# Kernel tuning notes

Measured on AMD Instinct MI355X. Metric: run time of the kernel, lower is better.

## Reference

```python
import jax, jax.numpy as jnp
import numpy as np

TEMPERATURE = 8.0  # sqrt(d_k), d_k=64
NEG_INF = -1e9

def setup_inputs() -> dict:
    key = jax.random.key(0)
    kq, kk, kv, km, kb = jax.random.split(key, 5)
    B, H, L, D = 2, 16, 2048, 64
    q = jax.random.normal(kq, (B, H, L, D), dtype=jnp.float32)
    k = jax.random.normal(kk, (B, H, L, D), dtype=jnp.float32)
    v = jax.random.normal(kv, (B, H, L, D), dtype=jnp.float32)
    mask = jax.random.randint(km, (B, 1, L, L), 0, 2, dtype=jnp.int32)
    pair_bias = jax.random.normal(kb, (B, 1, L, L), dtype=jnp.float32)
    return {"q": q, "k": k, "v": v, "mask": mask, "pair_bias": pair_bias}

def reference(q, k, v, mask, pair_bias):
    # scores: [B, H, Lq, Lk]
    attn = jnp.einsum('bhqd,bhkd->bhqk', q / TEMPERATURE, k)
    attn = attn + pair_bias  # broadcast over heads
    attn = jnp.where(mask == 0, NEG_INF, attn)
    attn = jax.nn.softmax(attn, axis=-1)
    # dropout prob is 0.0 -> identity
    head_output = jnp.einsum('bhqk,bhkd->bhqd', attn, v)
    return (head_output, attn)
```

## Files before the change

### kernel.cpp

```cpp
#include <hip/hip_runtime.h>

#define L  2048
#define D  64
#define NH 16
#define NB 2
#define KT 64
#define NT 32
#define LOG2E 1.44269504088896f

using half8   = _Float16 __attribute__((ext_vector_type(8)));
using half4v  = _Float16 __attribute__((ext_vector_type(4)));
using float4v = float    __attribute__((ext_vector_type(4)));
using int4v   = int      __attribute__((ext_vector_type(4)));

#define BAR()    asm volatile("s_barrier" ::: "memory")
#define WAITV(n) asm volatile("s_waitcnt vmcnt(" #n ")" ::: "memory")
#define WAITL()  asm volatile("s_waitcnt lgkmcnt(0)" ::: "memory")

__device__ __forceinline__ void gload16(const void* g, void* l) {
    __builtin_amdgcn_global_load_lds((const __attribute__((address_space(1))) void*)g,
                                     (__attribute__((address_space(3))) void*)l, 16, 0, 0);
}
__device__ __forceinline__ void gload4(const void* g, void* l) {
    __builtin_amdgcn_global_load_lds((const __attribute__((address_space(1))) void*)g,
                                     (__attribute__((address_space(3))) void*)l, 4, 0, 0);
}

__global__ __launch_bounds__(256) void prep_qk(const float* __restrict__ q,
                                               const float* __restrict__ k,
                                               _Float16* __restrict__ qh,
                                               _Float16* __restrict__ kh) {
    int i = (blockIdx.x * 256 + threadIdx.x) * 8;
    float4v a0 = *(const float4v*)(q + i);
    float4v a1 = *(const float4v*)(q + i + 4);
    float4v b0 = *(const float4v*)(k + i);
    float4v b1 = *(const float4v*)(k + i + 4);
    half8 qo, ko;
    const float s = 0.125f * LOG2E;
#pragma unroll
    for (int j = 0; j < 4; ++j) {
        qo[j]     = (_Float16)(a0[j] * s);
        qo[4 + j] = (_Float16)(a1[j] * s);
        ko[j]     = (_Float16)b0[j];
        ko[4 + j] = (_Float16)b1[j];
    }
    *(half8*)(qh + i) = qo;
    *(half8*)(kh + i) = ko;
}

__global__ __launch_bounds__(256) void prep_vt(const float* __restrict__ v,
                                               _Float16* __restrict__ vt) {
    __shared__ float tile[64][65];
    int bh = blockIdx.x >> 5;
    int l0 = (blockIdx.x & 31) * 64;
    const float* vb = v + (size_t)bh * L * D + (size_t)l0 * D;
    int row = threadIdx.x >> 2, c0 = (threadIdx.x & 3) * 16;
#pragma unroll
    for (int j = 0; j < 16; j += 4) {
        float4v t4 = *(const float4v*)(vb + row * D + c0 + j);
        tile[row][c0 + j + 0] = t4[0];
        tile[row][c0 + j + 1] = t4[1];
        tile[row][c0 + j + 2] = t4[2];
        tile[row][c0 + j + 3] = t4[3];
    }
    __syncthreads();
    int d = threadIdx.x >> 2, kbl = threadIdx.x & 3;
    int lq = kbl * 16;
    _Float16* ob = vt + (((size_t)bh * 128 + (l0 >> 4) + kbl) * 64 + d) * 16;
    half8 o0, o1;
#pragma unroll
    for (int j = 0; j < 8; ++j) {
        o0[j] = (_Float16)tile[lq + j][d];
        o1[j] = (_Float16)tile[lq + 8 + j][d];
    }
    *(half8*)(ob)     = o0;
    *(half8*)(ob + 8) = o1;
}

__global__ __launch_bounds__(256) void prep_mbh(const int* __restrict__ mask,
                                                const float* __restrict__ bias,
                                                _Float16* __restrict__ mbh) {
    int blk = blockIdx.x;
    int bq = blk >> 3, tg = blk & 7;
    int b  = bq >> 7, qt = bq & 127;
    int row = threadIdx.x >> 4;
    int c16 = threadIdx.x & 15;
    const int*   mrow = mask + ((size_t)b * L + qt * 16 + row) * L;
    const float* brow = bias + ((size_t)b * L + qt * 16 + row) * L;
    _Float16* obase = mbh + (size_t)bq * 32768 + (c16 >> 2) * 256 + row * 16 + (c16 & 3) * 4;
#pragma unroll
    for (int tt = 0; tt < 4; ++tt) {
        int t = tg * 4 + tt;
        int key = t * 64 + c16 * 4;
        int4v   m  = *(const int4v*)(mrow + key);
        float4v bb = *(const float4v*)(brow + key);
        half4v o;
        o[0] = m[0] ? (_Float16)(bb[0] * LOG2E) : (_Float16)(-1500.0f);
        o[1] = m[1] ? (_Float16)(bb[1] * LOG2E) : (_Float16)(-1500.0f);
        o[2] = m[2] ? (_Float16)(bb[2] * LOG2E) : (_Float16)(-1500.0f);
        o[3] = m[3] ? (_Float16)(bb[3] * LOG2E) : (_Float16)(-1500.0f);
        *(half4v*)(obase + t * 1024) = o;
    }
}

__global__ __launch_bounds__(256, 4) void attn_fused(const _Float16* __restrict__ qh,
                                                     const _Float16* __restrict__ kh,
                                                     const _Float16* __restrict__ vt,
                                                     const _Float16* __restrict__ mbh,
                                                     float* __restrict__ out_ho,
                                                     float* __restrict__ out_attn) {
    __shared__ __align__(16) char arena[36864];
    __shared__ float lpart[4][16];
    __shared__ float rls[16];

    int p  = blockIdx.x;
    int l  = (p & 7) * 512 + (p >> 3);
    int b  = l >> 11, h = (l >> 7) & 15, qt = l & 127;
    int bh = b * NH + h;
    int q0 = qt * 16;

    int tid = threadIdx.x, w = tid >> 6, lane = tid & 63;
    int cg = lane & 15, grp = lane >> 4;

    const _Float16* kg = kh  + (size_t)bh * L * D;
    const _Float16* vg = vt  + (size_t)bh * 131072;
    const _Float16* mg = mbh + (size_t)(b * 128 + qt) * 32768;
    const _Float16* qg = qh  + ((size_t)bh * L + q0) * D;

    half8 aq0 = *(const half8*)(qg + cg * D + grp * 8);
    half8 aq1 = *(const half8*)(qg + cg * D + 32 + grp * 8);

    _Float16* kbw = (_Float16*)(arena)         + w * 2048;
    _Float16* vbw = (_Float16*)(arena + 16384) + w * 2048;
    _Float16* mbw = (_Float16*)(arena + 32768) + w * 512;

    const int r8  = lane >> 3;
    const int kch = ((lane & 7) ^ r8) * 8;

    auto stage = [&](int t, int bs) {
        int kb = t * 4 + w;
        int k0 = kb * 16;
        _Float16* kd = kbw + bs * 1024;
        gload16(kg + (size_t)(k0 +     r8) * D + kch, kd);
        gload16(kg + (size_t)(k0 + 8 + r8) * D + kch, kd + 512);
        _Float16* vd = vbw + bs * 1024;
        const _Float16* vs = vg + (size_t)kb * 1024;
        gload16(vs + lane * 8, vd);
        gload16(vs + 512 + lane * 8, vd + 512);
        _Float16* md = mbw + bs * 256;
        const _Float16* ms = mg + (size_t)t * 1024 + w * 256;
        gload4(ms + lane * 2, md);
        gload4(ms + 128 + lane * 2, md + 128);
    };

    const int kro = cg * 64;
    const int ks0 = ((grp)     ^ (cg & 7)) * 8;
    const int ks1 = ((4 + grp) ^ (cg & 7)) * 8;
    const int mro = cg * 16 + grp * 4;
    const int vro = grp * 4;

    half4v puh[NT];
    float ls = 0.f;
    float4v oa0 = {0.f,0.f,0.f,0.f}, oa1 = {0.f,0.f,0.f,0.f};
    float4v oa2 = {0.f,0.f,0.f,0.f}, oa3 = {0.f,0.f,0.f,0.f};

    stage(0, 0);
#pragma unroll
    for (int t = 0; t < NT; ++t) {
        const int bs = t & 1;
        if (t + 1 < NT) { stage(t + 1, bs ^ 1); WAITV(6); }
        else            { WAITV(0); }
        const _Float16* kb = kbw + bs * 1024;
        const _Float16* mb = mbw + bs * 256;
        const _Float16* vb = vbw + bs * 1024;
        half8  bk0 = *(const half8*)(kb + kro + ks0);
        half8  bk1 = *(const half8*)(kb + kro + ks1);
        half4v m4  = *(const half4v*)(mb + mro);
        float4v acc;
        acc[0] = (float)m4[0]; acc[1] = (float)m4[1];
        acc[2] = (float)m4[2]; acc[3] = (float)m4[3];
        __builtin_amdgcn_s_setprio(1);
        acc = __builtin_amdgcn_mfma_f32_16x16x32_f16(bk0, aq0, acc, 0, 0, 0);
        acc = __builtin_amdgcn_mfma_f32_16x16x32_f16(bk1, aq1, acc, 0, 0, 0);
        __builtin_amdgcn_s_setprio(0);
        float e0 = exp2f(acc[0]), e1 = exp2f(acc[1]);
        float e2 = exp2f(acc[2]), e3 = exp2f(acc[3]);
        ls += (e0 + e1) + (e2 + e3);
        half4v ph;
        ph[0] = (_Float16)(e0 * 0.03125f); ph[1] = (_Float16)(e1 * 0.03125f);
        ph[2] = (_Float16)(e2 * 0.03125f); ph[3] = (_Float16)(e3 * 0.03125f);
        puh[t] = ph;
        half4v pv0 = *(const half4v*)(vb + (cg +  0) * 16 + vro);
        half4v pv1 = *(const half4v*)(vb + (cg + 16) * 16 + vro);
        half4v pv2 = *(const half4v*)(vb + (cg + 32) * 16 + vro);
        half4v pv3 = *(const half4v*)(vb + (cg + 48) * 16 + vro);
        __builtin_amdgcn_s_setprio(1);
        oa0 = __builtin_amdgcn_mfma_f32_16x16x16f16(ph, pv0, oa0, 0, 0, 0);
        oa1 = __builtin_amdgcn_mfma_f32_16x16x16f16(ph, pv1, oa1, 0, 0, 0);
        oa2 = __builtin_amdgcn_mfma_f32_16x16x16f16(ph, pv2, oa2, 0, 0, 0);
        oa3 = __builtin_amdgcn_mfma_f32_16x16x16f16(ph, pv3, oa3, 0, 0, 0);
        __builtin_amdgcn_s_setprio(0);
    }

    ls += __shfl_xor(ls, 16);
    ls += __shfl_xor(ls, 32);
    if (grp == 0) lpart[w][cg] = ls;
    __syncthreads();
    float lt = (lpart[0][cg] + lpart[1][cg]) + (lpart[2][cg] + lpart[3][cg]);
    float rl = 32.0f / lt;
    if (w == 0 && grp == 0) rls[cg] = rl;

    float* ored = (float*)(arena + 8192);
    float* orw  = ored + w * (16 * 68);
#pragma unroll
    for (int r = 0; r < 4; ++r) {
        orw[(grp * 4 + r) * 68 +  0 + cg] = oa0[r];
        orw[(grp * 4 + r) * 68 + 16 + cg] = oa1[r];
        orw[(grp * 4 + r) * 68 + 32 + cg] = oa2[r];
        orw[(grp * 4 + r) * 68 + 48 + cg] = oa3[r];
    }
    __syncthreads();
    {
        int qr = tid >> 4, d4 = (tid & 15) * 4;
        float4v s0 = *(const float4v*)(ored + 0 * 1088 + qr * 68 + d4);
        float4v s1 = *(const float4v*)(ored + 1 * 1088 + qr * 68 + d4);
        float4v s2 = *(const float4v*)(ored + 2 * 1088 + qr * 68 + d4);
        float4v s3 = *(const float4v*)(ored + 3 * 1088 + qr * 68 + d4);
        float rlo = rls[qr];
        float4v oo;
        oo[0] = ((s0[0] + s1[0]) + (s2[0] + s3[0])) * rlo;
        oo[1] = ((s0[1] + s1[1]) + (s2[1] + s3[1])) * rlo;
        oo[2] = ((s0[2] + s1[2]) + (s2[2] + s3[2])) * rlo;
        oo[3] = ((s0[3] + s1[3]) + (s2[3] + s3[3])) * rlo;
        __builtin_nontemporal_store(oo, (float4v*)(out_ho + ((size_t)bh * L + q0 + qr) * D + d4));
    }
    __syncthreads();

    float* arow = out_attn + ((size_t)bh * L + q0) * L;
    float* t32f = (float*)arena;
    const int gbase = w * 4 + grp;
    const int swrow = tid >> 4, jj = tid & 15;

#pragma unroll
    for (int ph = 0; ph < 8; ++ph) {
        float* tb = t32f + (ph & 1) * 4096;
#pragma unroll
        for (int i = 0; i < 4; ++i) {
            const int tt = ph * 4 + i;
            float4v pn;
            pn[0] = (float)puh[tt][0] * rl; pn[1] = (float)puh[tt][1] * rl;
            pn[2] = (float)puh[tt][2] * rl; pn[3] = (float)puh[tt][3] * rl;
            int g = (i * 16 + gbase) ^ (cg & 7);
            *(float4v*)(tb + cg * 256 + g * 4) = pn;
        }
        WAITL();
        BAR();
#pragma unroll
        for (int k = 0; k < 4; ++k) {
            int g = (jj + 16 * k) ^ (swrow & 7);
            float4v s = *(const float4v*)(tb + swrow * 256 + g * 4);
            __builtin_nontemporal_store(s,
                (float4v*)(arow + (size_t)swrow * L + ph * 256 + (jj + 16 * k) * 4));
        }
    }
}

extern "C" void kernel_launch(void* const* d_in, const int* in_sizes, int n_in,
                              void* d_out, int out_size, void* d_ws, size_t ws_size,
                              hipStream_t stream) {
    const float* q    = (const float*)d_in[0];
    const float* k    = (const float*)d_in[1];
    const float* v    = (const float*)d_in[2];
    const int*   mask = (const int*)d_in[3];
    const float* bias = (const float*)d_in[4];

    float* ho   = (float*)d_out;
    float* attn = (float*)d_out + (size_t)NB * NH * L * D;

    char* ws = (char*)d_ws;
    _Float16* qh  = (_Float16*)(ws);
    _Float16* kh  = (_Float16*)(ws + ((size_t)8  << 20));
    _Float16* vt  = (_Float16*)(ws + ((size_t)16 << 20));
    _Float16* mbh = (_Float16*)(ws + ((size_t)24 << 20));
    (void)in_sizes; (void)n_in; (void)out_size; (void)ws_size;

    prep_qk<<<2048, 256, 0, stream>>>(q, k, qh, kh);
    prep_vt<<<1024, 256, 0, stream>>>(v, vt);
    prep_mbh<<<2048, 256, 0, stream>>>(mask, bias, mbh);
    attn_fused<<<4096, 256, 0, stream>>>(qh, kh, vt, mbh, ho, attn);
}
```

Before: 192.1 us.

## Process 32 query rows per block to reuse staged K/V tiles

Each attention block now handles 32 query rows instead of 16. The K and V tiles staged in shared memory therefore feed two sets of MFMAs, which halves K/V global traffic and the block count. The mask/bias prep kernel writes a matching 32-row layout, so the mask tile can be loaded with 16-byte global-to-LDS loads instead of 4-byte ones. In exchange, register pressure roughly doubles (two puh arrays and eight accumulators), and launch bounds drop to 2 blocks per SM, which lowers occupancy.

```diff
diff --git a/kernel.cpp b/kernel.cpp
--- a/kernel.cpp
+++ b/kernel.cpp
@@ -20,10 +20,6 @@
 __device__ __forceinline__ void gload16(const void* g, void* l) {
     __builtin_amdgcn_global_load_lds((const __attribute__((address_space(1))) void*)g,
                                      (__attribute__((address_space(3))) void*)l, 16, 0, 0);
-}
-__device__ __forceinline__ void gload4(const void* g, void* l) {
-    __builtin_amdgcn_global_load_lds((const __attribute__((address_space(1))) void*)g,
-                                     (__attribute__((address_space(3))) void*)l, 4, 0, 0);
 }
 
 __global__ __launch_bounds__(256) void prep_qk(const float* __restrict__ q,
@@ -81,58 +77,64 @@
                                                 const float* __restrict__ bias,
                                                 _Float16* __restrict__ mbh) {
     int blk = blockIdx.x;
-    int bq = blk >> 3, tg = blk & 7;
-    int b  = bq >> 7, qt = bq & 127;
-    int row = threadIdx.x >> 4;
-    int c16 = threadIdx.x & 15;
-    const int*   mrow = mask + ((size_t)b * L + qt * 16 + row) * L;
-    const float* brow = bias + ((size_t)b * L + qt * 16 + row) * L;
-    _Float16* obase = mbh + (size_t)bq * 32768 + (c16 >> 2) * 256 + row * 16 + (c16 & 3) * 4;
-#pragma unroll
-    for (int tt = 0; tt < 4; ++tt) {
-        int t = tg * 4 + tt;
+    int bq = blk >> 4, tg = blk & 15;
+    int b  = bq >> 6, qt = bq & 63;
+    int row16 = threadIdx.x >> 4;
+    int c16   = threadIdx.x & 15;
+    int w = c16 >> 2, kl4 = (c16 & 3) * 4;
+#pragma unroll
+    for (int tt = 0; tt < 2; ++tt) {
+        int t = tg * 2 + tt;
         int key = t * 64 + c16 * 4;
-        int4v   m  = *(const int4v*)(mrow + key);
-        float4v bb = *(const float4v*)(brow + key);
-        half4v o;
-        o[0] = m[0] ? (_Float16)(bb[0] * LOG2E) : (_Float16)(-1500.0f);
-        o[1] = m[1] ? (_Float16)(bb[1] * LOG2E) : (_Float16)(-1500.0f);
-        o[2] = m[2] ? (_Float16)(bb[2] * LOG2E) : (_Float16)(-1500.0f);
-        o[3] = m[3] ? (_Float16)(bb[3] * LOG2E) : (_Float16)(-1500.0f);
-        *(half4v*)(obase + t * 1024) = o;
-    }
-}
-
-__global__ __launch_bounds__(256, 4) void attn_fused(const _Float16* __restrict__ qh,
+#pragma unroll
+        for (int rr = 0; rr < 2; ++rr) {
+            int row = row16 + rr * 16;
+            const int*   mrow = mask + ((size_t)b * L + qt * 32 + row) * L;
+            const float* brow = bias + ((size_t)b * L + qt * 32 + row) * L;
+            int4v   m  = *(const int4v*)(mrow + key);
+            float4v bb = *(const float4v*)(brow + key);
+            half4v o;
+            o[0] = m[0] ? (_Float16)(bb[0] * LOG2E) : (_Float16)(-1500.0f);
+            o[1] = m[1] ? (_Float16)(bb[1] * LOG2E) : (_Float16)(-1500.0f);
+            o[2] = m[2] ? (_Float16)(bb[2] * LOG2E) : (_Float16)(-1500.0f);
+            o[3] = m[3] ? (_Float16)(bb[3] * LOG2E) : (_Float16)(-1500.0f);
+            *(half4v*)(mbh + (size_t)bq * 65536 + t * 2048 + w * 512 + row * 16 + kl4) = o;
+        }
+    }
+}
+
+__global__ __launch_bounds__(256, 2) void attn_fused(const _Float16* __restrict__ qh,
                                                      const _Float16* __restrict__ kh,
                                                      const _Float16* __restrict__ vt,
                                                      const _Float16* __restrict__ mbh,
                                                      float* __restrict__ out_ho,
                                                      float* __restrict__ out_attn) {
-    __shared__ __align__(16) char arena[36864];
-    __shared__ float lpart[4][16];
-    __shared__ float rls[16];
+    __shared__ __align__(16) char arena[40960];
+    __shared__ float lpart[4][32];
+    __shared__ float rls[32];
 
     int p  = blockIdx.x;
-    int l  = (p & 7) * 512 + (p >> 3);
-    int b  = l >> 11, h = (l >> 7) & 15, qt = l & 127;
+    int l  = (p & 7) * 256 + (p >> 3);
+    int b  = l >> 10, h = (l >> 6) & 15, qt = l & 63;
     int bh = b * NH + h;
-    int q0 = qt * 16;
+    int q0 = qt * 32;
 
     int tid = threadIdx.x, w = tid >> 6, lane = tid & 63;
     int cg = lane & 15, grp = lane >> 4;
 
     const _Float16* kg = kh  + (size_t)bh * L * D;
     const _Float16* vg = vt  + (size_t)bh * 131072;
-    const _Float16* mg = mbh + (size_t)(b * 128 + qt) * 32768;
+    const _Float16* mg = mbh + (size_t)(b * 64 + qt) * 65536;
     const _Float16* qg = qh  + ((size_t)bh * L + q0) * D;
 
-    half8 aq0 = *(const half8*)(qg + cg * D + grp * 8);
-    half8 aq1 = *(const half8*)(qg + cg * D + 32 + grp * 8);
+    half8 aqA0 = *(const half8*)(qg + cg * D + grp * 8);
+    half8 aqA1 = *(const half8*)(qg + cg * D + 32 + grp * 8);
+    half8 aqB0 = *(const half8*)(qg + (16 + cg) * D + grp * 8);
+    half8 aqB1 = *(const half8*)(qg + (16 + cg) * D + 32 + grp * 8);
 
     _Float16* kbw = (_Float16*)(arena)         + w * 2048;
     _Float16* vbw = (_Float16*)(arena + 16384) + w * 2048;
-    _Float16* mbw = (_Float16*)(arena + 32768) + w * 512;
+    _Float16* mbw = (_Float16*)(arena + 32768) + w * 1024;
 
     const int r8  = lane >> 3;
     const int kch = ((lane & 7) ^ r8) * 8;
@@ -147,120 +149,149 @@
         const _Float16* vs = vg + (size_t)kb * 1024;
         gload16(vs + lane * 8, vd);
         gload16(vs + 512 + lane * 8, vd + 512);
-        _Float16* md = mbw + bs * 256;
-        const _Float16* ms = mg + (size_t)t * 1024 + w * 256;
-        gload4(ms + lane * 2, md);
-        gload4(ms + 128 + lane * 2, md + 128);
+        _Float16* md = mbw + bs * 512;
+        gload16(mg + (size_t)t * 2048 + w * 512 + lane * 8, md);
     };
 
-    const int kro = cg * 64;
-    const int ks0 = ((grp)     ^ (cg & 7)) * 8;
-    const int ks1 = ((4 + grp) ^ (cg & 7)) * 8;
-    const int mro = cg * 16 + grp * 4;
-    const int vro = grp * 4;
-
-    half4v puh[NT];
-    float ls = 0.f;
-    float4v oa0 = {0.f,0.f,0.f,0.f}, oa1 = {0.f,0.f,0.f,0.f};
-    float4v oa2 = {0.f,0.f,0.f,0.f}, oa3 = {0.f,0.f,0.f,0.f};
+    const int kro  = cg * 64;
+    const int ks0  = ((grp)     ^ (cg & 7)) * 8;
+    const int ks1  = ((4 + grp) ^ (cg & 7)) * 8;
+    const int mroA = cg * 16 + grp * 4;
+    const int mroB = mroA + 256;
+    const int vro  = grp * 4;
+
+    half4v puhA[NT], puhB[NT];
+    float lsA = 0.f, lsB = 0.f;
+    float4v oaA0 = {0,0,0,0}, oaA1 = {0,0,0,0}, oaA2 = {0,0,0,0}, oaA3 = {0,0,0,0};
+    float4v oaB0 = {0,0,0,0}, oaB1 = {0,0,0,0}, oaB2 = {0,0,0,0}, oaB3 = {0,0,0,0};
 
     stage(0, 0);
 #pragma unroll
     for (int t = 0; t < NT; ++t) {
         const int bs = t & 1;
-        if (t + 1 < NT) { stage(t + 1, bs ^ 1); WAITV(6); }
+        if (t + 1 < NT) { stage(t + 1, bs ^ 1); WAITV(5); }
         else            { WAITV(0); }
         const _Float16* kb = kbw + bs * 1024;
-        const _Float16* mb = mbw + bs * 256;
+        const _Float16* mb = mbw + bs * 512;
         const _Float16* vb = vbw + bs * 1024;
         half8  bk0 = *(const half8*)(kb + kro + ks0);
         half8  bk1 = *(const half8*)(kb + kro + ks1);
-        half4v m4  = *(const half4v*)(mb + mro);
-        float4v acc;
-        acc[0] = (float)m4[0]; acc[1] = (float)m4[1];
-        acc[2] = (float)m4[2]; acc[3] = (float)m4[3];
+        half4v m4A = *(const half4v*)(mb + mroA);
+        half4v m4B = *(const half4v*)(mb + mroB);
+        float4v accA, accB;
+        accA[0] = (float)m4A[0]; accA[1] = (float)m4A[1];
+        accA[2] = (float)m4A[2]; accA[3] = (float)m4A[3];
+        accB[0] = (float)m4B[0]; accB[1] = (float)m4B[1];
+        accB[2] = (float)m4B[2]; accB[3] = (float)m4B[3];
         __builtin_amdgcn_s_setprio(1);
-        acc = __builtin_amdgcn_mfma_f32_16x16x32_f16(bk0, aq0, acc, 0, 0, 0);
-        acc = __builtin_amdgcn_mfma_f32_16x16x32_f16(bk1, aq1, acc, 0, 0, 0);
+        accA = __builtin_amdgcn_mfma_f32_16x16x32_f16(bk0, aqA0, accA, 0, 0, 0);
+        accA = __builtin_amdgcn_mfma_f32_16x16x32_f16(bk1, aqA1, accA, 0, 0, 0);
+        accB = __builtin_amdgcn_mfma_f32_16x16x32_f16(bk0, aqB0, accB, 0, 0, 0);
+        accB = __builtin_amdgcn_mfma_f32_16x16x32_f16(bk1, aqB1, accB, 0, 0, 0);
         __builtin_amdgcn_s_setprio(0);
-        float e0 = exp2f(acc[0]), e1 = exp2f(acc[1]);
-        float e2 = exp2f(acc[2]), e3 = exp2f(acc[3]);
-        ls += (e0 + e1) + (e2 + e3);
-        half4v ph;
-        ph[0] = (_Float16)(e0 * 0.03125f); ph[1] = (_Float16)(e1 * 0.03125f);
-        ph[2] = (_Float16)(e2 * 0.03125f); ph[3] = (_Float16)(e3 * 0.03125f);
-        puh[t] = ph;
+        float eA0 = exp2f(accA[0]), eA1 = exp2f(accA[1]);
+        float eA2 = exp2f(accA[2]), eA3 = exp2f(accA[3]);
+        float eB0 = exp2f(accB[0]), eB1 = exp2f(accB[1]);
+        float eB2 = exp2f(accB[2]), eB3 = exp2f(accB[3]);
+        lsA += (eA0 + eA1) + (eA2 + eA3);
+        lsB += (eB0 + eB1) + (eB2 + eB3);
+        half4v phA, phB;
+        phA[0] = (_Float16)(eA0 * 0.03125f); phA[1] = (_Float16)(eA1 * 0.03125f);
+        phA[2] = (_Float16)(eA2 * 0.03125f); phA[3] = (_Float16)(eA3 * 0.03125f);
+        phB[0] = (_Float16)(eB0 * 0.03125f); phB[1] = (_Float16)(eB1 * 0.03125f);
+        phB[2] = (_Float16)(eB2 * 0.03125f); phB[3] = (_Float16)(eB3 * 0.03125f);
+        puhA[t] = phA;
+        puhB[t] = phB;
         half4v pv0 = *(const half4v*)(vb + (cg +  0) * 16 + vro);
         half4v pv1 = *(const half4v*)(vb + (cg + 16) * 16 + vro);
         half4v pv2 = *(const half4v*)(vb + (cg + 32) * 16 + vro);
         half4v pv3 = *(const half4v*)(vb + (cg + 48) * 16 + vro);
         __builtin_amdgcn_s_setprio(1);
-        oa0 = __builtin_amdgcn_mfma_f32_16x16x16f16(ph, pv0, oa0, 0, 0, 0);
-        oa1 = __builtin_amdgcn_mfma_f32_16x16x16f16(ph, pv1, oa1, 0, 0, 0);
-        oa2 = __builtin_amdgcn_mfma_f32_16x16x16f16(ph, pv2, oa2, 0, 0, 0);
-        oa3 = __builtin_amdgcn_mfma_f32_16x16x16f16(ph, pv3, oa3, 0, 0, 0);
+        oaA0 = __builtin_amdgcn_mfma_f32_16x16x16f16(phA, pv0, oaA0, 0, 0, 0);
+        oaA1 = __builtin_amdgcn_mfma_f32_16x16x16f16(phA, pv1, oaA1, 0, 0, 0);
+        oaA2 = __builtin_amdgcn_mfma_f32_16x16x16f16(phA, pv2, oaA2, 0, 0, 0);
+        oaA3 = __builtin_amdgcn_mfma_f32_16x16x16f16(phA, pv3, oaA3, 0, 0, 0);
+        oaB0 = __builtin_amdgcn_mfma_f32_16x16x16f16(phB, pv0, oaB0, 0, 0, 0);
+        oaB1 = __builtin_amdgcn_mfma_f32_16x16x16f16(phB, pv1, oaB1, 0, 0, 0);
+        oaB2 = __builtin_amdgcn_mfma_f32_16x16x16f16(phB, pv2, oaB2, 0, 0, 0);
+        oaB3 = __builtin_amdgcn_mfma_f32_16x16x16f16(phB, pv3, oaB3, 0, 0, 0);
         __builtin_amdgcn_s_setprio(0);
     }
 
-    ls += __shfl_xor(ls, 16);
-    ls += __shfl_xor(ls, 32);
-    if (grp == 0) lpart[w][cg] = ls;
+    lsA += __shfl_xor(lsA, 16);
+    lsA += __shfl_xor(lsA, 32);
+    lsB += __shfl_xor(lsB, 16);
+    lsB += __shfl_xor(lsB, 32);
+    if (grp == 0) { lpart[w][cg] = lsA; lpart[w][16 + cg] = lsB; }
     __syncthreads();
-    float lt = (lpart[0][cg] + lpart[1][cg]) + (lpart[2][cg] + lpart[3][cg]);
-    float rl = 32.0f / lt;
-    if (w == 0 && grp == 0) rls[cg] = rl;
-
-    float* ored = (float*)(arena + 8192);
-    float* orw  = ored + w * (16 * 68);
+    float ltA = (lpart[0][cg] + lpart[1][cg]) + (lpart[2][cg] + lpart[3][cg]);
+    float ltB = (lpart[0][16 + cg] + lpart[1][16 + cg]) + (lpart[2][16 + cg] + lpart[3][16 + cg]);
+    float rlA = 32.0f / ltA;
+    float rlB = 32.0f / ltB;
+    if (w == 0 && grp == 0) { rls[cg] = rlA; rls[16 + cg] = rlB; }
+
+    float* ored = (float*)arena;
+    float* orw  = ored + w * 2176;
 #pragma unroll
     for (int r = 0; r < 4; ++r) {
-        orw[(grp * 4 + r) * 68 +  0 + cg] = oa0[r];
-        orw[(grp * 4 + r) * 68 + 16 + cg] = oa1[r];
-        orw[(grp * 4 + r) * 68 + 32 + cg] = oa2[r];
-        orw[(grp * 4 + r) * 68 + 48 + cg] = oa3[r];
+        orw[(grp * 4 + r) * 68 +  0 + cg] = oaA0[r];
+        orw[(grp * 4 + r) * 68 + 16 + cg] = oaA1[r];
+        orw[(grp * 4 + r) * 68 + 32 + cg] = oaA2[r];
+        orw[(grp * 4 + r) * 68 + 48 + cg] = oaA3[r];
+        orw[(16 + grp * 4 + r) * 68 +  0 + cg] = oaB0[r];
+        orw[(16 + grp * 4 + r) * 68 + 16 + cg] = oaB1[r];
+        orw[(16 + grp * 4 + r) * 68 + 32 + cg] = oaB2[r];
+        orw[(16 + grp * 4 + r) * 68 + 48 + cg] = oaB3[r];
     }
     __syncthreads();
     {
-        int qr = tid >> 4, d4 = (tid & 15) * 4;
-        float4v s0 = *(const float4v*)(ored + 0 * 1088 + qr * 68 + d4);
-        float4v s1 = *(const float4v*)(ored + 1 * 1088 + qr * 68 + d4);
-        float4v s2 = *(const float4v*)(ored + 2 * 1088 + qr * 68 + d4);
-        float4v s3 = *(const float4v*)(ored + 3 * 1088 + qr * 68 + d4);
+        int qr = tid >> 3, d8 = (tid & 7) * 8;
         float rlo = rls[qr];
-        float4v oo;
-        oo[0] = ((s0[0] + s1[0]) + (s2[0] + s3[0])) * rlo;
-        oo[1] = ((s0[1] + s1[1]) + (s2[1] + s3[1])) * rlo;
-        oo[2] = ((s0[2] + s1[2]) + (s2[2] + s3[2])) * rlo;
-        oo[3] = ((s0[3] + s1[3]) + (s2[3] + s3[3])) * rlo;
-        __builtin_nontemporal_store(oo, (float4v*)(out_ho + ((size_t)bh * L + q0 + qr) * D + d4));
+        float4v u0 = {0,0,0,0}, u1 = {0,0,0,0};
+#pragma unroll
+        for (int ww = 0; ww < 4; ++ww) {
+            float4v a = *(const float4v*)(ored + ww * 2176 + qr * 68 + d8);
+            float4v c = *(const float4v*)(ored + ww * 2176 + qr * 68 + d8 + 4);
+            u0[0] += a[0]; u0[1] += a[1]; u0[2] += a[2]; u0[3] += a[3];
+            u1[0] += c[0]; u1[1] += c[1]; u1[2] += c[2]; u1[3] += c[3];
+        }
+        u0[0] *= rlo; u0[1] *= rlo; u0[2] *= rlo; u0[3] *= rlo;
+        u1[0] *= rlo; u1[1] *= rlo; u1[2] *= rlo; u1[3] *= rlo;
+        float* ob = out_ho + ((size_t)bh * L + q0 + qr) * D + d8;
+        __builtin_nontemporal_store(u0, (float4v*)(ob));
+        __builtin_nontemporal_store(u1, (float4v*)(ob + 4));
     }
     __syncthreads();
 
-    float* arow = out_attn + ((size_t)bh * L + q0) * L;
-    float* t32f = (float*)arena;
+    float* arow0 = out_attn + ((size_t)bh * L + q0) * L;
+    float* t32f  = (float*)arena;
     const int gbase = w * 4 + grp;
     const int swrow = tid >> 4, jj = tid & 15;
 
 #pragma unroll
-    for (int ph = 0; ph < 8; ++ph) {
+    for (int ph = 0; ph < 16; ++ph) {
+        const int rg = ph & 1, tg = ph >> 1;
         float* tb = t32f + (ph & 1) * 4096;
+        const float rr = (rg == 0) ? rlA : rlB;
 #pragma unroll
         for (int i = 0; i < 4; ++i) {
-            const int tt = ph * 4 + i;
+            const int tt = tg * 4 + i;
+            const half4v ph4 = (rg == 0) ? puhA[tt] : puhB[tt];
             float4v pn;
-            pn[0] = (float)puh[tt][0] * rl; pn[1] = (float)puh[tt][1] * rl;
-            pn[2] = (float)puh[tt][2] * rl; pn[3] = (float)puh[tt][3] * rl;
+            pn[0] = (float)ph4[0] * rr; pn[1] = (float)ph4[1] * rr;
+            pn[2] = (float)ph4[2] * rr; pn[3] = (float)ph4[3] * rr;
             int g = (i * 16 + gbase) ^ (cg & 7);
             *(float4v*)(tb + cg * 256 + g * 4) = pn;
         }
         WAITL();
         BAR();
+        float* arow = arow0 + (size_t)(rg * 16) * L;
 #pragma unroll
         for (int k = 0; k < 4; ++k) {
             int g = (jj + 16 * k) ^ (swrow & 7);
             float4v s = *(const float4v*)(tb + swrow * 256 + g * 4);
             __builtin_nontemporal_store(s,
-                (float4v*)(arow + (size_t)swrow * L + ph * 256 + (jj + 16 * k) * 4));
+                (float4v*)(arow + (size_t)swrow * L + tg * 256 + (jj + 16 * k) * 4));
         }
     }
 }
@@ -287,5 +318,5 @@
     prep_qk<<<2048, 256, 0, stream>>>(q, k, qh, kh);
     prep_vt<<<1024, 256, 0, stream>>>(v, vt);
     prep_mbh<<<2048, 256, 0, stream>>>(mask, bias, mbh);
-    attn_fused<<<4096, 256, 0, stream>>>(qh, kh, vt, mbh, ho, attn);
-}
+    attn_fused<<<2048, 256, 0, stream>>>(qh, kh, vt, mbh, ho, attn);
+}
```

Measured after the change: 194.8 us. About the same (+1.4%).

## Process two query tiles per block, overlapping first tile's attn store with second compute

Applied to the files above, without the earlier changes.

Each block now handles 32 query rows as two sequential 16-row tiles, halving the grid. The normalized attention-matrix stores for the first tile are interleaved into the main loop of the second tile, so output write traffic overlaps with MFMA compute. Mask/bias values are loaded straight into registers with a one-step prefetch instead of being staged through LDS, which frees LDS for a transpose buffer. In exchange the block runs longer with more register pressure and extra barriers, and the grid has half as many blocks.

```diff
diff --git a/kernel.cpp b/kernel.cpp
--- a/kernel.cpp
+++ b/kernel.cpp
@@ -20,10 +20,6 @@
 __device__ __forceinline__ void gload16(const void* g, void* l) {
     __builtin_amdgcn_global_load_lds((const __attribute__((address_space(1))) void*)g,
                                      (__attribute__((address_space(3))) void*)l, 16, 0, 0);
-}
-__device__ __forceinline__ void gload4(const void* g, void* l) {
-    __builtin_amdgcn_global_load_lds((const __attribute__((address_space(1))) void*)g,
-                                     (__attribute__((address_space(3))) void*)l, 4, 0, 0);
 }
 
 __global__ __launch_bounds__(256) void prep_qk(const float* __restrict__ q,
@@ -109,30 +105,28 @@
                                                      const _Float16* __restrict__ mbh,
                                                      float* __restrict__ out_ho,
                                                      float* __restrict__ out_attn) {
-    __shared__ __align__(16) char arena[36864];
-    __shared__ float lpart[4][16];
-    __shared__ float rls[16];
+    __shared__ __align__(16) char arena[40960];
 
     int p  = blockIdx.x;
-    int l  = (p & 7) * 512 + (p >> 3);
-    int b  = l >> 11, h = (l >> 7) & 15, qt = l & 127;
+    int l  = (p & 7) * 256 + (p >> 3);
+    int b  = l >> 10, h = (l >> 6) & 15, qp = l & 63;
     int bh = b * NH + h;
-    int q0 = qt * 16;
+    int q0 = qp * 32;
 
     int tid = threadIdx.x, w = tid >> 6, lane = tid & 63;
     int cg = lane & 15, grp = lane >> 4;
 
-    const _Float16* kg = kh  + (size_t)bh * L * D;
-    const _Float16* vg = vt  + (size_t)bh * 131072;
-    const _Float16* mg = mbh + (size_t)(b * 128 + qt) * 32768;
-    const _Float16* qg = qh  + ((size_t)bh * L + q0) * D;
-
-    half8 aq0 = *(const half8*)(qg + cg * D + grp * 8);
-    half8 aq1 = *(const half8*)(qg + cg * D + 32 + grp * 8);
-
-    _Float16* kbw = (_Float16*)(arena)         + w * 2048;
-    _Float16* vbw = (_Float16*)(arena + 16384) + w * 2048;
-    _Float16* mbw = (_Float16*)(arena + 32768) + w * 512;
+    const _Float16* kg  = kh  + (size_t)bh * L * D;
+    const _Float16* vg  = vt  + (size_t)bh * 131072;
+    const _Float16* mg0 = mbh + (size_t)(b * 128 + qp * 2) * 32768;
+    const _Float16* mg1 = mg0 + 32768;
+    const _Float16* qg  = qh  + ((size_t)bh * L + q0) * D;
+
+    _Float16* kbw  = (_Float16*)(arena)         + w * 2048;
+    _Float16* vbw  = (_Float16*)(arena + 16384) + w * 2048;
+    float*    t32B = (float*)(arena + 32768);
+    float*    lpart = (float*)(arena + 32768);
+    float*    rls   = (float*)(arena + 33024);
 
     const int r8  = lane >> 3;
     const int kch = ((lane & 7) ^ r8) * 8;
@@ -147,38 +141,31 @@
         const _Float16* vs = vg + (size_t)kb * 1024;
         gload16(vs + lane * 8, vd);
         gload16(vs + 512 + lane * 8, vd + 512);
-        _Float16* md = mbw + bs * 256;
-        const _Float16* ms = mg + (size_t)t * 1024 + w * 256;
-        gload4(ms + lane * 2, md);
-        gload4(ms + 128 + lane * 2, md + 128);
     };
 
-    const int kro = cg * 64;
-    const int ks0 = ((grp)     ^ (cg & 7)) * 8;
-    const int ks1 = ((4 + grp) ^ (cg & 7)) * 8;
-    const int mro = cg * 16 + grp * 4;
-    const int vro = grp * 4;
+    const int kro  = cg * 64;
+    const int ks0  = ((grp)     ^ (cg & 7)) * 8;
+    const int ks1  = ((4 + grp) ^ (cg & 7)) * 8;
+    const int vro  = grp * 4;
+    const int moff = w * 256 + cg * 16 + grp * 4;
+    const int srow = tid >> 4, sjj = tid & 15;
+
+    half8 aq0 = *(const half8*)(qg + cg * D + grp * 8);
+    half8 aq1 = *(const half8*)(qg + cg * D + 32 + grp * 8);
 
     half4v puh[NT];
     float ls = 0.f;
-    float4v oa0 = {0.f,0.f,0.f,0.f}, oa1 = {0.f,0.f,0.f,0.f};
-    float4v oa2 = {0.f,0.f,0.f,0.f}, oa3 = {0.f,0.f,0.f,0.f};
-
-    stage(0, 0);
-#pragma unroll
-    for (int t = 0; t < NT; ++t) {
+    float4v oa0 = {0,0,0,0}, oa1 = {0,0,0,0}, oa2 = {0,0,0,0}, oa3 = {0,0,0,0};
+
+    auto body = [&](int t, half4v mcur) {
         const int bs = t & 1;
-        if (t + 1 < NT) { stage(t + 1, bs ^ 1); WAITV(6); }
-        else            { WAITV(0); }
         const _Float16* kb = kbw + bs * 1024;
-        const _Float16* mb = mbw + bs * 256;
         const _Float16* vb = vbw + bs * 1024;
-        half8  bk0 = *(const half8*)(kb + kro + ks0);
-        half8  bk1 = *(const half8*)(kb + kro + ks1);
-        half4v m4  = *(const half4v*)(mb + mro);
+        half8 bk0 = *(const half8*)(kb + kro + ks0);
+        half8 bk1 = *(const half8*)(kb + kro + ks1);
         float4v acc;
-        acc[0] = (float)m4[0]; acc[1] = (float)m4[1];
-        acc[2] = (float)m4[2]; acc[3] = (float)m4[3];
+        acc[0] = (float)mcur[0]; acc[1] = (float)mcur[1];
+        acc[2] = (float)mcur[2]; acc[3] = (float)mcur[3];
         __builtin_amdgcn_s_setprio(1);
         acc = __builtin_amdgcn_mfma_f32_16x16x32_f16(bk0, aq0, acc, 0, 0, 0);
         acc = __builtin_amdgcn_mfma_f32_16x16x32_f16(bk1, aq1, acc, 0, 0, 0);
@@ -200,27 +187,18 @@
         oa2 = __builtin_amdgcn_mfma_f32_16x16x16f16(ph, pv2, oa2, 0, 0, 0);
         oa3 = __builtin_amdgcn_mfma_f32_16x16x16f16(ph, pv3, oa3, 0, 0, 0);
         __builtin_amdgcn_s_setprio(0);
-    }
-
-    ls += __shfl_xor(ls, 16);
-    ls += __shfl_xor(ls, 32);
-    if (grp == 0) lpart[w][cg] = ls;
-    __syncthreads();
-    float lt = (lpart[0][cg] + lpart[1][cg]) + (lpart[2][cg] + lpart[3][cg]);
-    float rl = 32.0f / lt;
-    if (w == 0 && grp == 0) rls[cg] = rl;
-
-    float* ored = (float*)(arena + 8192);
-    float* orw  = ored + w * (16 * 68);
-#pragma unroll
-    for (int r = 0; r < 4; ++r) {
-        orw[(grp * 4 + r) * 68 +  0 + cg] = oa0[r];
-        orw[(grp * 4 + r) * 68 + 16 + cg] = oa1[r];
-        orw[(grp * 4 + r) * 68 + 32 + cg] = oa2[r];
-        orw[(grp * 4 + r) * 68 + 48 + cg] = oa3[r];
-    }
-    __syncthreads();
-    {
+    };
+
+    auto ho_epilogue = [&](int row0, float* ored) {
+        float* orw = ored + w * 1088;
+#pragma unroll
+        for (int r = 0; r < 4; ++r) {
+            orw[(grp * 4 + r) * 68 +  0 + cg] = oa0[r];
+            orw[(grp * 4 + r) * 68 + 16 + cg] = oa1[r];
+            orw[(grp * 4 + r) * 68 + 32 + cg] = oa2[r];
+            orw[(grp * 4 + r) * 68 + 48 + cg] = oa3[r];
+        }
+        __syncthreads();
         int qr = tid >> 4, d4 = (tid & 15) * 4;
         float4v s0 = *(const float4v*)(ored + 0 * 1088 + qr * 68 + d4);
         float4v s1 = *(const float4v*)(ored + 1 * 1088 + qr * 68 + d4);
@@ -232,24 +210,105 @@
         oo[1] = ((s0[1] + s1[1]) + (s2[1] + s3[1])) * rlo;
         oo[2] = ((s0[2] + s1[2]) + (s2[2] + s3[2])) * rlo;
         oo[3] = ((s0[3] + s1[3]) + (s2[3] + s3[3])) * rlo;
-        __builtin_nontemporal_store(oo, (float4v*)(out_ho + ((size_t)bh * L + q0 + qr) * D + d4));
-    }
-    __syncthreads();
-
-    float* arow = out_attn + ((size_t)bh * L + q0) * L;
-    float* t32f = (float*)arena;
+        __builtin_nontemporal_store(oo, (float4v*)(out_ho + ((size_t)bh * L + row0 + qr) * D + d4));
+    };
+
+    half4v mcur, mnxt;
+    stage(0, 0);
+    mcur = *(const half4v*)(mg0 + moff);
+#pragma unroll
+    for (int t = 0; t < NT; ++t) {
+        if (t + 1 < NT) {
+            stage(t + 1, (t & 1) ^ 1);
+            mnxt = *(const half4v*)(mg0 + (size_t)(t + 1) * 1024 + moff);
+            WAITV(5);
+        } else { WAITV(0); }
+        body(t, mcur);
+        mcur = mnxt;
+    }
+    ls += __shfl_xor(ls, 16);
+    ls += __shfl_xor(ls, 32);
+    if (grp == 0) lpart[w * 16 + cg] = ls;
+    __syncthreads();
+    float rl0 = 32.0f / ((lpart[cg] + lpart[16 + cg]) + (lpart[32 + cg] + lpart[48 + cg]));
+    if (w == 0 && grp == 0) rls[cg] = rl0;
+    __syncthreads();
+    ho_epilogue(q0, (float*)arena);
+    __syncthreads();
+
+    aq0 = *(const half8*)(qg + (16 + cg) * D + grp * 8);
+    aq1 = *(const half8*)(qg + (16 + cg) * D + 32 + grp * 8);
+    oa0 = oa1 = oa2 = oa3 = float4v{0, 0, 0, 0};
+    ls = 0.f;
+    float* arow0 = out_attn + ((size_t)bh * L + q0) * L;
+
+    stage(0, 0);
+    mcur = *(const half4v*)(mg1 + moff);
+#pragma unroll
+    for (int j = 0; j < 16; ++j) {
+#pragma unroll
+        for (int tl = 0; tl < 2; ++tl) {
+            half4v p4 = puh[2 * j + tl];
+            float4v pn;
+            pn[0] = (float)p4[0] * rl0; pn[1] = (float)p4[1] * rl0;
+            pn[2] = (float)p4[2] * rl0; pn[3] = (float)p4[3] * rl0;
+            int g = tl * 16 + w * 4 + grp;
+            *(float4v*)(t32B + cg * 128 + ((g ^ (cg & 7)) * 4)) = pn;
+        }
+        WAITL();
+        BAR();
+#pragma unroll
+        for (int k = 0; k < 2; ++k) {
+            int gr = (k * 16 + sjj) ^ (srow & 7);
+            float4v s = *(const float4v*)(t32B + srow * 128 + gr * 4);
+            __builtin_nontemporal_store(s,
+                (float4v*)(arow0 + (size_t)srow * L + j * 128 + (k * 16 + sjj) * 4));
+        }
+        BAR();
+        {
+            int t = 2 * j;
+            if (t + 1 < NT) {
+                stage(t + 1, (t & 1) ^ 1);
+                mnxt = *(const half4v*)(mg1 + (size_t)(t + 1) * 1024 + moff);
+                WAITV(7);
+            } else { WAITV(0); }
+            body(t, mcur);
+            mcur = mnxt;
+        }
+        {
+            int t = 2 * j + 1;
+            if (t + 1 < NT) {
+                stage(t + 1, (t & 1) ^ 1);
+                mnxt = *(const half4v*)(mg1 + (size_t)(t + 1) * 1024 + moff);
+                WAITV(5);
+            } else { WAITV(0); }
+            body(t, mcur);
+            mcur = mnxt;
+        }
+    }
+    ls += __shfl_xor(ls, 16);
+    ls += __shfl_xor(ls, 32);
+    if (grp == 0) lpart[w * 16 + cg] = ls;
+    __syncthreads();
+    float rl1 = 32.0f / ((lpart[cg] + lpart[16 + cg]) + (lpart[32 + cg] + lpart[48 + cg]));
+    if (w == 0 && grp == 0) rls[cg] = rl1;
+    __syncthreads();
+    ho_epilogue(q0 + 16, (float*)arena);
+    __syncthreads();
+
+    float* arow1 = out_attn + ((size_t)bh * L + q0 + 16) * L;
+    float* t32C  = (float*)arena;
     const int gbase = w * 4 + grp;
-    const int swrow = tid >> 4, jj = tid & 15;
-
 #pragma unroll
     for (int ph = 0; ph < 8; ++ph) {
-        float* tb = t32f + (ph & 1) * 4096;
+        float* tb = t32C + (ph & 1) * 4096;
 #pragma unroll
         for (int i = 0; i < 4; ++i) {
             const int tt = ph * 4 + i;
+            half4v p4 = puh[tt];
             float4v pn;
-            pn[0] = (float)puh[tt][0] * rl; pn[1] = (float)puh[tt][1] * rl;
-            pn[2] = (float)puh[tt][2] * rl; pn[3] = (float)puh[tt][3] * rl;
+            pn[0] = (float)p4[0] * rl1; pn[1] = (float)p4[1] * rl1;
+            pn[2] = (float)p4[2] * rl1; pn[3] = (float)p4[3] * rl1;
             int g = (i * 16 + gbase) ^ (cg & 7);
             *(float4v*)(tb + cg * 256 + g * 4) = pn;
         }
@@ -257,10 +316,10 @@
         BAR();
 #pragma unroll
         for (int k = 0; k < 4; ++k) {
-            int g = (jj + 16 * k) ^ (swrow & 7);
-            float4v s = *(const float4v*)(tb + swrow * 256 + g * 4);
+            int g = (sjj + 16 * k) ^ (srow & 7);
+            float4v s = *(const float4v*)(tb + srow * 256 + g * 4);
             __builtin_nontemporal_store(s,
-                (float4v*)(arow + (size_t)swrow * L + ph * 256 + (jj + 16 * k) * 4));
+                (float4v*)(arow1 + (size_t)srow * L + ph * 256 + (sjj + 16 * k) * 4));
         }
     }
 }
@@ -287,5 +346,5 @@
     prep_qk<<<2048, 256, 0, stream>>>(q, k, qh, kh);
     prep_vt<<<1024, 256, 0, stream>>>(v, vt);
     prep_mbh<<<2048, 256, 0, stream>>>(mask, bias, mbh);
-    attn_fused<<<4096, 256, 0, stream>>>(qh, kh, vt, mbh, ho, attn);
-}
+    attn_fused<<<2048, 256, 0, stream>>>(qh, kh, vt, mbh, ho, attn);
+}
```

After: 580.5 us. 3.02x slower.
